# Kernel optimization log

Measured on AMD Instinct MI355X. Metric: run time of the kernel, lower is better.

The kernel has to match this reference:

```python
import jax, jax.numpy as jnp
import numpy as np

N, IPI, OPI, OPO = 20000, 128, 64, 16

def setup_inputs() -> dict:
    key = jax.random.key(0)
    k1, k2, k3, k4 = jax.random.split(key, 4)
    admat = jax.random.uniform(k1, (N, N), dtype=jnp.float32)
    features = jax.random.normal(k2, (N, IPI), dtype=jnp.float32)
    W1 = jax.random.normal(k3, (IPI, OPI), dtype=jnp.float32) * (1.0 / np.sqrt(IPI))
    W2 = jax.random.normal(k4, (OPI, OPO), dtype=jnp.float32) * (1.0 / np.sqrt(OPI))
    return {"admat": admat, "features": features, "W1": W1, "W2": W2}

def reference(admat, features, W1, W2):
    # layer1: A @ (X @ W1), thin-first ordering to minimize FLOPs/traffic
    h = jax.nn.relu(admat @ (features @ W1))          # [N, OPI]
    logits = admat @ (h @ W2)                          # [N, OPO]
    return jax.nn.softmax(logits, axis=1)
```

## Files before the change

### kernel.cpp

```cpp
#include <hip/hip_runtime.h>
#include <hip/hip_bf16.h>

#define NROWS 20000
#define IPI 128
#define OPI 64
#define OPO 16
#define BK 256

typedef __attribute__((ext_vector_type(8))) short bf16x8;
typedef __attribute__((ext_vector_type(4))) float f32x4;
typedef __attribute__((ext_vector_type(2))) unsigned int u32x2;

static __device__ __forceinline__ unsigned short f2bf(float f) {
    __hip_bfloat16 h = __float2bfloat16(f);
    return *reinterpret_cast<unsigned short*>(&h);
}
static __device__ __forceinline__ unsigned pk2(float a, float b) {
    return (unsigned)f2bf(a) | ((unsigned)f2bf(b) << 16);
}

__global__ __launch_bounds__(256)
void k_xw1(const float* __restrict__ X, const float* __restrict__ W1,
           unsigned short* __restrict__ Bt) {
    __shared__ float w1[IPI * OPI];
    const int t = threadIdx.x;
    for (int i = t * 4; i < IPI * OPI; i += 1024)
        *(float4*)&w1[i] = *(const float4*)&W1[i];
    __syncthreads();

    const int r  = blockIdx.x * 16 + (t >> 4);
    const int c4 = (t & 15) * 4;
    const float* xr = X + (size_t)r * IPI;
    float4 acc = make_float4(0.f, 0.f, 0.f, 0.f);
    #pragma unroll 8
    for (int k = 0; k < IPI; ++k) {
        const float x = xr[k];
        const float4 w = *(const float4*)&w1[k * OPI + c4];
        acc.x = fmaf(x, w.x, acc.x);
        acc.y = fmaf(x, w.y, acc.y);
        acc.z = fmaf(x, w.z, acc.z);
        acc.w = fmaf(x, w.w, acc.w);
    }
    Bt[(size_t)(c4 + 0) * NROWS + r] = f2bf(acc.x);
    Bt[(size_t)(c4 + 1) * NROWS + r] = f2bf(acc.y);
    Bt[(size_t)(c4 + 2) * NROWS + r] = f2bf(acc.z);
    Bt[(size_t)(c4 + 3) * NROWS + r] = f2bf(acc.w);
}

__global__ __launch_bounds__(256)
void k_gemm1(const float* __restrict__ A, const unsigned short* __restrict__ Bt,
             float* __restrict__ Out, int KC) {
    __shared__ unsigned short As[64 * BK];
    __shared__ unsigned short Bs[64 * BK];
    const int t    = threadIdx.x;
    const int lane = t & 63;
    const int wid  = t >> 6;
    const int lrow = lane & 15;
    const int lk   = lane >> 4;
    const int brow    = blockIdx.x * 64;
    const int k_begin = blockIdx.y * KC;
    const int k_end   = min(NROWS, k_begin + KC);

    const int sc_c = lane >> 1;
    const int sc_h = (lane & 1) * 4;

    f32x4 acc[4];
    #pragma unroll
    for (int n = 0; n < 4; ++n) acc[n] = (f32x4){0.f, 0.f, 0.f, 0.f};

    for (int kt = k_begin; kt < k_end; kt += BK) {
        const int  kg  = kt + lane * 4;
        const bool kok = kg < k_end;

        f32x4 va[16];
        u32x2 vb[16];
        #pragma unroll
        for (int i = 0; i < 16; ++i) {
            const int grow = brow + wid * 16 + i;
            va[i] = (f32x4){0.f, 0.f, 0.f, 0.f};
            if (kok && grow < NROWS)
                va[i] = __builtin_nontemporal_load(
                    (const f32x4*)(A + (size_t)grow * NROWS + kg));
            vb[i] = (u32x2){0u, 0u};
            if (kok)
                vb[i] = *(const u32x2*)(Bt + (size_t)(wid * 16 + i) * NROWS + kg);
        }
        #pragma unroll
        for (int i = 0; i < 16; ++i) {
            const int r = wid * 16 + i;
            u32x2 u;
            u[0] = pk2(va[i][0], va[i][1]);
            u[1] = pk2(va[i][2], va[i][3]);
            const int slot = (sc_c ^ (r & 7)) * 8 + sc_h;
            *(u32x2*)&As[r * BK + slot] = u;
            *(u32x2*)&Bs[r * BK + slot] = vb[i];
        }
        __syncthreads();

        #pragma unroll
        for (int h = 0; h < 8; ++h) {
            const int c  = h * 4 + lk;
            const int sc = (c & ~7) | ((c & 7) ^ (lrow & 7));
            const bf16x8 a = *(const bf16x8*)&As[(wid * 16 + lrow) * BK + sc * 8];
            #pragma unroll
            for (int n = 0; n < 4; ++n) {
                const bf16x8 b = *(const bf16x8*)&Bs[(n * 16 + lrow) * BK + sc * 8];
                acc[n] = __builtin_amdgcn_mfma_f32_16x16x32_bf16(a, b, acc[n], 0, 0, 0);
            }
        }
        __syncthreads();
    }

    float* outp = Out + (size_t)blockIdx.y * NROWS * OPI;
    const int r0 = (lane >> 4) * 4;
    #pragma unroll
    for (int n = 0; n < 4; ++n)
        #pragma unroll
        for (int r = 0; r < 4; ++r) {
            const int grow = brow + wid * 16 + r0 + r;
            if (grow < NROWS)
                outp[(size_t)grow * OPI + n * 16 + lrow] = acc[n][r];
        }
}

__global__ __launch_bounds__(256)
void k_hw2(const float* __restrict__ Hpart, const float* __restrict__ W2,
           unsigned short* __restrict__ Zt, int S1) {
    __shared__ float w2[OPI * OPO];
    __shared__ float hs[16 * 68];
    const int t = threadIdx.x;
    if (t * 4 < OPI * OPO)
        *(float4*)&w2[t * 4] = *(const float4*)&W2[t * 4];

    const int r  = t >> 4;
    const int c4 = (t & 15) * 4;
    const size_t rowg = (size_t)blockIdx.x * 16 + r;

    float4 h = make_float4(0.f, 0.f, 0.f, 0.f);
    for (int s = 0; s < S1; ++s) {
        const float4 v = *(const float4*)&Hpart[((size_t)s * NROWS + rowg) * OPI + c4];
        h.x += v.x; h.y += v.y; h.z += v.z; h.w += v.w;
    }
    hs[r * 68 + c4 + 0] = fmaxf(h.x, 0.f);
    hs[r * 68 + c4 + 1] = fmaxf(h.y, 0.f);
    hs[r * 68 + c4 + 2] = fmaxf(h.z, 0.f);
    hs[r * 68 + c4 + 3] = fmaxf(h.w, 0.f);
    __syncthreads();

    const int c = t & 15;
    float z = 0.f;
    #pragma unroll 8
    for (int k = 0; k < OPI; ++k)
        z = fmaf(hs[r * 68 + k], w2[k * OPO + c], z);
    Zt[(size_t)c * NROWS + rowg] = f2bf(z);
}

__global__ __launch_bounds__(256)
void k_gemm2(const float* __restrict__ A, const unsigned short* __restrict__ Zt,
             float* __restrict__ Out, int KC) {
    __shared__ unsigned short As[64 * BK];
    __shared__ unsigned short Bs[16 * BK];
    const int t    = threadIdx.x;
    const int lane = t & 63;
    const int wid  = t >> 6;
    const int lrow = lane & 15;
    const int lk   = lane >> 4;
    const int brow    = blockIdx.x * 64;
    const int k_begin = blockIdx.y * KC;
    const int k_end   = min(NROWS, k_begin + KC);

    const int sc_c = lane >> 1;
    const int sc_h = (lane & 1) * 4;

    f32x4 acc = (f32x4){0.f, 0.f, 0.f, 0.f};

    for (int kt = k_begin; kt < k_end; kt += BK) {
        const int  kg  = kt + lane * 4;
        const bool kok = kg < k_end;

        f32x4 va[16];
        #pragma unroll
        for (int i = 0; i < 16; ++i) {
            const int grow = brow + wid * 16 + i;
            va[i] = (f32x4){0.f, 0.f, 0.f, 0.f};
            if (kok && grow < NROWS)
                va[i] = __builtin_nontemporal_load(
                    (const f32x4*)(A + (size_t)grow * NROWS + kg));
        }
        u32x2 vz[4];
        #pragma unroll
        for (int i = 0; i < 4; ++i) {
            vz[i] = (u32x2){0u, 0u};
            if (kok)
                vz[i] = *(const u32x2*)(Zt + (size_t)(wid * 4 + i) * NROWS + kg);
        }
        #pragma unroll
        for (int i = 0; i < 16; ++i) {
            const int r = wid * 16 + i;
            u32x2 u;
            u[0] = pk2(va[i][0], va[i][1]);
            u[1] = pk2(va[i][2], va[i][3]);
            *(u32x2*)&As[r * BK + (sc_c ^ (r & 7)) * 8 + sc_h] = u;
        }
        #pragma unroll
        for (int i = 0; i < 4; ++i) {
            const int c = wid * 4 + i;
            *(u32x2*)&Bs[c * BK + (sc_c ^ (c & 7)) * 8 + sc_h] = vz[i];
        }
        __syncthreads();

        #pragma unroll
        for (int h = 0; h < 8; ++h) {
            const int c  = h * 4 + lk;
            const int sc = (c & ~7) | ((c & 7) ^ (lrow & 7));
            const bf16x8 a = *(const bf16x8*)&As[(wid * 16 + lrow) * BK + sc * 8];
            const bf16x8 b = *(const bf16x8*)&Bs[lrow * BK + sc * 8];
            acc = __builtin_amdgcn_mfma_f32_16x16x32_bf16(a, b, acc, 0, 0, 0);
        }
        __syncthreads();
    }

    float* outp = Out + (size_t)blockIdx.y * NROWS * OPO;
    const int r0 = (lane >> 4) * 4;
    #pragma unroll
    for (int r = 0; r < 4; ++r) {
        const int grow = brow + wid * 16 + r0 + r;
        if (grow < NROWS) outp[(size_t)grow * OPO + lrow] = acc[r];
    }
}

__global__ __launch_bounds__(256)
void k_softmax(const float* __restrict__ Lpart, float* __restrict__ out, int S2) {
    const int t = threadIdx.x;
    const size_t base = (size_t)blockIdx.x * 256;
    float v = 0.f;
    for (int s = 0; s < S2; ++s)
        v += Lpart[(size_t)s * NROWS * OPO + base + t];
    float m = v;
    #pragma unroll
    for (int d = 8; d >= 1; d >>= 1) m = fmaxf(m, __shfl_xor(m, d, 16));
    const float e = expf(v - m);
    float sum = e;
    #pragma unroll
    for (int d = 8; d >= 1; d >>= 1) sum += __shfl_xor(sum, d, 16);
    out[base + t] = e / sum;
}

extern "C" void kernel_launch(void* const* d_in, const int* in_sizes, int n_in,
                              void* d_out, int out_size, void* d_ws, size_t ws_size,
                              hipStream_t stream) {
    const float* A  = (const float*)d_in[0];
    const float* X  = (const float*)d_in[1];
    const float* W1 = (const float*)d_in[2];
    const float* W2 = (const float*)d_in[3];
    float* out = (float*)d_out;

    auto al = [](size_t x) { return (x + 255) & ~(size_t)255; };
    const size_t bt_b = al((size_t)OPI * NROWS * 2);
    const size_t zt_b = al((size_t)OPO * NROWS * 2);

    int S1 = 8, S2 = 8;
    auto need = [&](int s1, int s2) {
        return bt_b + zt_b +
               ((size_t)s1 * NROWS * OPI + (size_t)s2 * NROWS * OPO) * sizeof(float);
    };
    while ((S1 > 1 || S2 > 1) && need(S1, S2) > ws_size) {
        if (S1 > 1) S1 >>= 1;
        if (S2 > 1) S2 >>= 1;
    }

    char* p = (char*)d_ws;
    unsigned short* Bt = (unsigned short*)p;
    unsigned short* Zt = (unsigned short*)(p + bt_b);
    float* H = (float*)(p + bt_b + zt_b);
    float* L = H + (size_t)S1 * NROWS * OPI;

    const int MT  = (NROWS + 63) / 64;
    const int KC1 = ((((NROWS + S1 - 1) / S1) + BK - 1) / BK) * BK;
    const int KC2 = ((((NROWS + S2 - 1) / S2) + BK - 1) / BK) * BK;

    k_xw1<<<dim3(NROWS / 16), 256, 0, stream>>>(X, W1, Bt);
    k_gemm1<<<dim3(MT, S1), 256, 0, stream>>>(A, Bt, H, KC1);
    k_hw2<<<dim3(NROWS / 16), 256, 0, stream>>>(H, W2, Zt, S1);
    k_gemm2<<<dim3(MT, S2), 256, 0, stream>>>(A, Zt, L, KC2);
    k_softmax<<<dim3(NROWS * OPO / 256), 256, 0, stream>>>(L, out, S2);
}
```

Measured before the change: 622.0 us.

## Write FP8 copy of adjacency in gemm1 and run gemm2 with FP8 MFMA

While gemm1 streams the fp32 adjacency matrix, it also writes a packed FP8 copy to workspace. gemm2 then reads that 1-byte copy instead of the 4-byte original and uses FP8 MFMA, with Z scaled by 0.25 into FP8 and the logits rescaled in softmax. The aim is to cut gemm2's dominant HBM traffic from 1.6GB to 0.4GB. The cost is an extra 400MB write in gemm1, a large workspace requirement, and reduced precision from FP8 rounding of both operands.

```diff
diff --git a/kernel.cpp b/kernel.cpp
--- a/kernel.cpp
+++ b/kernel.cpp
@@ -6,6 +6,7 @@
 #define OPI 64
 #define OPO 16
 #define BK 256
+#define BK2 512
 
 typedef __attribute__((ext_vector_type(8))) short bf16x8;
 typedef __attribute__((ext_vector_type(4))) float f32x4;
@@ -17,6 +18,14 @@
 }
 static __device__ __forceinline__ unsigned pk2(float a, float b) {
     return (unsigned)f2bf(a) | ((unsigned)f2bf(b) << 16);
+}
+static __device__ __forceinline__ unsigned pk4_fp8(float a, float b, float c, float d) {
+    int v = __builtin_amdgcn_cvt_pk_fp8_f32(a, b, 0, false);
+    v = __builtin_amdgcn_cvt_pk_fp8_f32(c, d, v, true);
+    return (unsigned)v;
+}
+static __device__ __forceinline__ unsigned char f2fp8(float a) {
+    return (unsigned char)(pk4_fp8(a, 0.f, 0.f, 0.f) & 0xff);
 }
 
 __global__ __launch_bounds__(256)
@@ -49,7 +58,7 @@
 
 __global__ __launch_bounds__(256)
 void k_gemm1(const float* __restrict__ A, const unsigned short* __restrict__ Bt,
-             float* __restrict__ Out, int KC) {
+             float* __restrict__ Out, unsigned char* __restrict__ A8, int KC) {
     __shared__ unsigned short As[64 * BK];
     __shared__ unsigned short Bs[64 * BK];
     const int t    = threadIdx.x;
@@ -88,12 +97,17 @@
         #pragma unroll
         for (int i = 0; i < 16; ++i) {
             const int r = wid * 16 + i;
+            const int grow = brow + r;
             u32x2 u;
             u[0] = pk2(va[i][0], va[i][1]);
             u[1] = pk2(va[i][2], va[i][3]);
             const int slot = (sc_c ^ (r & 7)) * 8 + sc_h;
             *(u32x2*)&As[r * BK + slot] = u;
             *(u32x2*)&Bs[r * BK + slot] = vb[i];
+            if (kok && grow < NROWS)
+                __builtin_nontemporal_store(
+                    pk4_fp8(va[i][0], va[i][1], va[i][2], va[i][3]),
+                    (unsigned*)(A8 + (size_t)grow * NROWS + kg));
         }
         __syncthreads();
 
@@ -125,7 +139,7 @@
 
 __global__ __launch_bounds__(256)
 void k_hw2(const float* __restrict__ Hpart, const float* __restrict__ W2,
-           unsigned short* __restrict__ Zt, int S1) {
+           unsigned char* __restrict__ Zt8, int S1) {
     __shared__ float w2[OPI * OPO];
     __shared__ float hs[16 * 68];
     const int t = threadIdx.x;
@@ -152,14 +166,15 @@
     #pragma unroll 8
     for (int k = 0; k < OPI; ++k)
         z = fmaf(hs[r * 68 + k], w2[k * OPO + c], z);
-    Zt[(size_t)c * NROWS + rowg] = f2bf(z);
-}
-
-__global__ __launch_bounds__(256)
-void k_gemm2(const float* __restrict__ A, const unsigned short* __restrict__ Zt,
+    Zt8[(size_t)c * NROWS + rowg] = f2fp8(z * 0.25f);
+}
+
+__global__ __launch_bounds__(256)
+void k_gemm2(const unsigned char* __restrict__ A8,
+             const unsigned char* __restrict__ Zt8,
              float* __restrict__ Out, int KC) {
-    __shared__ unsigned short As[64 * BK];
-    __shared__ unsigned short Bs[16 * BK];
+    __shared__ unsigned char As[64 * BK2];
+    __shared__ unsigned char Bs[16 * BK2];
     const int t    = threadIdx.x;
     const int lane = t & 63;
     const int wid  = t >> 6;
@@ -169,53 +184,51 @@
     const int k_begin = blockIdx.y * KC;
     const int k_end   = min(NROWS, k_begin + KC);
 
-    const int sc_c = lane >> 1;
-    const int sc_h = (lane & 1) * 4;
-
     f32x4 acc = (f32x4){0.f, 0.f, 0.f, 0.f};
 
-    for (int kt = k_begin; kt < k_end; kt += BK) {
-        const int  kg  = kt + lane * 4;
-        const bool kok = kg < k_end;
-
-        f32x4 va[16];
+    for (int kt = k_begin; kt < k_end; kt += BK2) {
+        const int  kgA = kt + lane * 8;
+        const bool okA = kgA < k_end;
+        u32x2 va[16];
         #pragma unroll
         for (int i = 0; i < 16; ++i) {
             const int grow = brow + wid * 16 + i;
-            va[i] = (f32x4){0.f, 0.f, 0.f, 0.f};
-            if (kok && grow < NROWS)
+            va[i] = (u32x2){0u, 0u};
+            if (okA && grow < NROWS)
                 va[i] = __builtin_nontemporal_load(
-                    (const f32x4*)(A + (size_t)grow * NROWS + kg));
-        }
-        u32x2 vz[4];
-        #pragma unroll
-        for (int i = 0; i < 4; ++i) {
-            vz[i] = (u32x2){0u, 0u};
-            if (kok)
-                vz[i] = *(const u32x2*)(Zt + (size_t)(wid * 4 + i) * NROWS + kg);
+                    (const u32x2*)(A8 + (size_t)grow * NROWS + kgA));
         }
         #pragma unroll
         for (int i = 0; i < 16; ++i) {
-            const int r = wid * 16 + i;
-            u32x2 u;
-            u[0] = pk2(va[i][0], va[i][1]);
-            u[1] = pk2(va[i][2], va[i][3]);
-            *(u32x2*)&As[r * BK + (sc_c ^ (r & 7)) * 8 + sc_h] = u;
-        }
-        #pragma unroll
-        for (int i = 0; i < 4; ++i) {
-            const int c = wid * 4 + i;
-            *(u32x2*)&Bs[c * BK + (sc_c ^ (c & 7)) * 8 + sc_h] = vz[i];
+            const int r    = wid * 16 + i;
+            const int c    = lane >> 1;
+            const int half = (lane & 1) * 8;
+            const int sc   = (c & ~7) | ((c & 7) ^ (r & 7));
+            *(u32x2*)&As[r * BK2 + sc * 16 + half] = va[i];
+        }
+        {
+            const int col = t >> 4;
+            const int off = (t & 15) * 32;
+            const int kg  = kt + off;
+            const unsigned char* zp = Zt8 + (size_t)col * NROWS + kg;
+            uint4 v0 = make_uint4(0, 0, 0, 0), v1 = make_uint4(0, 0, 0, 0);
+            if (kg < k_end)      v0 = *(const uint4*)zp;
+            if (kg + 16 < k_end) v1 = *(const uint4*)(zp + 16);
+            const int c0 = off >> 4, c1 = c0 + 1;
+            *(uint4*)&Bs[col * BK2 + ((c0 & ~7) | ((c0 & 7) ^ (col & 7))) * 16] = v0;
+            *(uint4*)&Bs[col * BK2 + ((c1 & ~7) | ((c1 & 7) ^ (col & 7))) * 16] = v1;
         }
         __syncthreads();
 
         #pragma unroll
-        for (int h = 0; h < 8; ++h) {
-            const int c  = h * 4 + lk;
-            const int sc = (c & ~7) | ((c & 7) ^ (lrow & 7));
-            const bf16x8 a = *(const bf16x8*)&As[(wid * 16 + lrow) * BK + sc * 8];
-            const bf16x8 b = *(const bf16x8*)&Bs[lrow * BK + sc * 8];
-            acc = __builtin_amdgcn_mfma_f32_16x16x32_bf16(a, b, acc, 0, 0, 0);
+        for (int h = 0; h < 16; ++h) {
+            const int k0   = h * 32 + lk * 8;
+            const int c    = k0 >> 4;
+            const int half = k0 & 8;
+            const int sc   = (c & ~7) | ((c & 7) ^ (lrow & 7));
+            const long long a = *(const long long*)&As[(wid * 16 + lrow) * BK2 + sc * 16 + half];
+            const long long b = *(const long long*)&Bs[lrow * BK2 + sc * 16 + half];
+            acc = __builtin_amdgcn_mfma_f32_16x16x32_fp8_fp8(a, b, acc, 0, 0, 0);
         }
         __syncthreads();
     }
@@ -236,6 +249,7 @@
     float v = 0.f;
     for (int s = 0; s < S2; ++s)
         v += Lpart[(size_t)s * NROWS * OPO + base + t];
+    v *= 4.f;
     float m = v;
     #pragma unroll
     for (int d = 8; d >= 1; d >>= 1) m = fmaxf(m, __shfl_xor(m, d, 16));
@@ -256,12 +270,13 @@
     float* out = (float*)d_out;
 
     auto al = [](size_t x) { return (x + 255) & ~(size_t)255; };
+    const size_t a8_b = al((size_t)NROWS * NROWS);
     const size_t bt_b = al((size_t)OPI * NROWS * 2);
-    const size_t zt_b = al((size_t)OPO * NROWS * 2);
+    const size_t z8_b = al((size_t)OPO * NROWS);
 
     int S1 = 8, S2 = 8;
     auto need = [&](int s1, int s2) {
-        return bt_b + zt_b +
+        return a8_b + bt_b + z8_b +
                ((size_t)s1 * NROWS * OPI + (size_t)s2 * NROWS * OPO) * sizeof(float);
     };
     while ((S1 > 1 || S2 > 1) && need(S1, S2) > ws_size) {
@@ -270,18 +285,19 @@
     }
 
     char* p = (char*)d_ws;
-    unsigned short* Bt = (unsigned short*)p;
-    unsigned short* Zt = (unsigned short*)(p + bt_b);
-    float* H = (float*)(p + bt_b + zt_b);
+    unsigned char*  A8  = (unsigned char*)p;
+    unsigned short* Bt  = (unsigned short*)(p + a8_b);
+    unsigned char*  Zt8 = (unsigned char*)(p + a8_b + bt_b);
+    float* H = (float*)(p + a8_b + bt_b + z8_b);
     float* L = H + (size_t)S1 * NROWS * OPI;
 
     const int MT  = (NROWS + 63) / 64;
-    const int KC1 = ((((NROWS + S1 - 1) / S1) + BK - 1) / BK) * BK;
-    const int KC2 = ((((NROWS + S2 - 1) / S2) + BK - 1) / BK) * BK;
+    const int KC1 = ((((NROWS + S1 - 1) / S1) + BK  - 1) / BK ) * BK;
+    const int KC2 = ((((NROWS + S2 - 1) / S2) + BK2 - 1) / BK2) * BK2;
 
     k_xw1<<<dim3(NROWS / 16), 256, 0, stream>>>(X, W1, Bt);
-    k_gemm1<<<dim3(MT, S1), 256, 0, stream>>>(A, Bt, H, KC1);
-    k_hw2<<<dim3(NROWS / 16), 256, 0, stream>>>(H, W2, Zt, S1);
-    k_gemm2<<<dim3(MT, S2), 256, 0, stream>>>(A, Zt, L, KC2);
+    k_gemm1<<<dim3(MT, S1), 256, 0, stream>>>(A, Bt, H, A8, KC1);
+    k_hw2<<<dim3(NROWS / 16), 256, 0, stream>>>(H, W2, Zt8, S1);
+    k_gemm2<<<dim3(MT, S2), 256, 0, stream>>>(A8, Zt8, L, KC2);
     k_softmax<<<dim3(NROWS * OPO / 256), 256, 0, stream>>>(L, out, S2);
 }
```

Measured after the change: 592.4 us. 1.05x faster.
